# Performance work log

Measured on AMD Instinct MI355X. Metric: run time of the kernel, lower is better.

The kernel has to match this reference:

```python
import jax, jax.numpy as jnp
import numpy as np

WS = 6        # window size -> N = 36 tokens per window
HEADS = 16

def _rel_index(ws):
    coords = np.stack(np.meshgrid(np.arange(ws), np.arange(ws), indexing='ij')).reshape(2, -1)
    rel = coords[:, :, None] - coords[:, None, :] + (ws - 1)
    return jnp.asarray(rel[0] * (2 * ws - 1) + rel[1])  # (N, N) int

REL_IDX = _rel_index(WS)

def _ln(x, g, b, eps=1e-5):
    m = x.mean(-1, keepdims=True)
    v = x.var(-1, keepdims=True)
    return (x - m) / jnp.sqrt(v + eps) * g + b

def setup_inputs() -> dict:
    key = jax.random.key(0)
    ks = jax.random.split(key, 6)
    B, H, W, C = 16, 96, 96, 512
    hid = 4 * C
    s = 0.02
    return {
        'x': jax.random.normal(ks[0], (B, H, W, C), jnp.float32),
        'w_qkv': jax.random.normal(ks[1], (C, 3 * C), jnp.float32) * s,
        'w_proj': jax.random.normal(ks[2], (C, C), jnp.float32) * s,
        'b_proj': jnp.zeros((C,), jnp.float32),
        'rel_bias': jax.random.normal(ks[3], ((2 * WS - 1) ** 2, HEADS), jnp.float32) * s,
        'ln1_g': jnp.ones((C,), jnp.float32), 'ln1_b': jnp.zeros((C,), jnp.float32),
        'ln2_g': jnp.ones((C,), jnp.float32), 'ln2_b': jnp.zeros((C,), jnp.float32),
        'w_fc1': jax.random.normal(ks[4], (C, hid), jnp.float32) * s,
        'b_fc1': jnp.zeros((hid,), jnp.float32),
        'w_fc2': jax.random.normal(ks[5], (hid, C), jnp.float32) * s,
        'b_fc2': jnp.zeros((C,), jnp.float32),
    }

def reference(x, w_qkv, w_proj, b_proj, rel_bias, ln1_g, ln1_b, ln2_g, ln2_b, w_fc1, b_fc1, w_fc2, b_fc2):
    B, H, W, C = x.shape
    h, d, N = HEADS, C // HEADS, WS * WS
    nh, nw = H // WS, W // WS
    # window partition: (B,H,W,C) -> (B*nh*nw, N, C)
    xw = x.reshape(B, nh, WS, nw, WS, C).transpose(0, 1, 3, 2, 4, 5).reshape(B * nh * nw, N, C)
    xn = _ln(xw, ln1_g, ln1_b)
    qkv = xn @ w_qkv
    q, k, v = jnp.split(qkv, 3, axis=-1)
    to_heads = lambda t: t.reshape(-1, N, h, d).transpose(0, 2, 1, 3)  # (B_, h, N, d)
    q = to_heads(q) * (d ** -0.5)
    k = to_heads(k)
    v = to_heads(v)
    attn = jnp.einsum('bhnd,bhmd->bhnm', q, k)
    bias = rel_bias[REL_IDX.reshape(-1)].reshape(N, N, h).transpose(2, 0, 1)  # (h, N, N)
    attn = jax.nn.softmax(attn + bias[None], axis=-1)
    o = jnp.einsum('bhnm,bhmd->bhnd', attn, v).transpose(0, 2, 1, 3).reshape(-1, N, C)
    o = o @ w_proj + b_proj
    # un-window; NOTE: source has no residual around attention (x is replaced)
    x2 = o.reshape(B, nh, nw, WS, WS, C).transpose(0, 1, 3, 2, 4, 5).reshape(B, H, W, C)
    xm = _ln(x2, ln2_g, ln2_b)
    mlp = jax.nn.gelu(xm @ w_fc1 + b_fc1, approximate=False) @ w_fc2 + b_fc2
    return x2 + mlp
```

## Files before the change

kernel.cpp:

```cpp
#include <hip/hip_runtime.h>
#include <stdint.h>

#define TOK 147456
#define CCH 512

typedef __attribute__((ext_vector_type(8))) short short8;
typedef __attribute__((ext_vector_type(4))) float f32x4;

struct alignas(8) US4 { unsigned short a, b, c, d; };

typedef __attribute__((address_space(3))) void lds_void;
typedef const __attribute__((address_space(1))) void gbl_void;

__device__ inline void gload16(const void* g, void* l) {
    __builtin_amdgcn_global_load_lds((gbl_void*)g, (lds_void*)l, 16, 0, 0);
}

__device__ inline unsigned short f2bf(float f) {
    union { float f; unsigned u; } v{f};
    unsigned r = v.u + 0x7fffu + ((v.u >> 16) & 1u);
    return (unsigned short)(r >> 16);
}
__device__ inline float bf2f(unsigned short h) {
    union { unsigned u; float f; } v; v.u = ((unsigned)h) << 16; return v.f;
}

__global__ void wprep(const float* __restrict__ in, unsigned short* __restrict__ out,
                      int K, int N) {
    int idx = blockIdx.x * 256 + threadIdx.x;
    if (idx >= K * N) return;
    int k = idx / N, n = idx % N;
    out[(size_t)n * K + k] = f2bf(in[idx]);
}

__global__ void biasprep(const float* __restrict__ rb, float* __restrict__ bb) {
    int idx = blockIdx.x * 256 + threadIdx.x;
    if (idx >= 16 * 48 * 48) return;
    int h = idx / 2304, rem = idx % 2304, r = rem / 48, c = rem % 48;
    float v = -1e9f;
    if (r < 36 && c < 36) {
        int dy = r / 6 - c / 6 + 5;
        int dx = r % 6 - c % 6 + 5;
        v = rb[(dy * 11 + dx) * 16 + h];
    }
    bb[idx] = v;
}

__global__ __launch_bounds__(256) void ln_k(const float* __restrict__ x,
                                            const float* __restrict__ g,
                                            const float* __restrict__ b,
                                            unsigned short* __restrict__ out, int ntok) {
    int lane = threadIdx.x & 63;
    int tok = blockIdx.x * 4 + (threadIdx.x >> 6);
    if (tok >= ntok) return;
    const float4* xr = (const float4*)(x + (size_t)tok * CCH);
    float4 v0 = xr[lane], v1 = xr[lane + 64];
    float s  = v0.x + v0.y + v0.z + v0.w + v1.x + v1.y + v1.z + v1.w;
    float s2 = v0.x*v0.x + v0.y*v0.y + v0.z*v0.z + v0.w*v0.w
             + v1.x*v1.x + v1.y*v1.y + v1.z*v1.z + v1.w*v1.w;
#pragma unroll
    for (int off = 32; off; off >>= 1) { s += __shfl_xor(s, off); s2 += __shfl_xor(s2, off); }
    float mean = s * (1.f / 512.f);
    float var  = s2 * (1.f / 512.f) - mean * mean;
    float inv  = rsqrtf(var + 1e-5f);
    const float4* gp = (const float4*)g;
    const float4* bp = (const float4*)b;
    float4 g0 = gp[lane], g1 = gp[lane + 64], b0 = bp[lane], b1 = bp[lane + 64];
    US4 o0, o1;
    o0.a = f2bf((v0.x - mean) * inv * g0.x + b0.x);
    o0.b = f2bf((v0.y - mean) * inv * g0.y + b0.y);
    o0.c = f2bf((v0.z - mean) * inv * g0.z + b0.z);
    o0.d = f2bf((v0.w - mean) * inv * g0.w + b0.w);
    o1.a = f2bf((v1.x - mean) * inv * g1.x + b1.x);
    o1.b = f2bf((v1.y - mean) * inv * g1.y + b1.y);
    o1.c = f2bf((v1.z - mean) * inv * g1.z + b1.z);
    o1.d = f2bf((v1.w - mean) * inv * g1.w + b1.w);
    unsigned short* op = out + (size_t)tok * CCH;
    *(US4*)(op + 4 * lane)       = o0;
    *(US4*)(op + 256 + 4 * lane) = o1;
}

__global__ __launch_bounds__(256) void attn_mfma(const unsigned short* __restrict__ qkv,
                                                 const float* __restrict__ biasb,
                                                 unsigned short* __restrict__ o) {
    __shared__ __align__(16) unsigned short p_lds[4][48 * 64];
    __shared__ __align__(16) unsigned short v_lds[4][32 * 64];

    int tid  = threadIdx.x;
    int wv   = tid >> 6;
    int lane = tid & 63;
    int l15  = lane & 15;
    int g    = lane >> 4;

    int wid = blockIdx.x * 4 + wv;
    int h   = wid & 15;
    int win = wid >> 4;
    int img  = win >> 8;
    int wrow = (win >> 4) & 15;
    int wcol = win & 15;
    int tok_base = (img * 96 + wrow * 6) * 96 + wcol * 6;

    unsigned short* pw = p_lds[wv];
    unsigned short* vw = v_lds[wv];

    #define TOKOF(r) (tok_base + (r) + 90 * ((r) / 6))

    short8 z8 = {};
    for (int e = lane; e < 224; e += 64) {
        if (e < 128) {
            int ch = e >> 2, kst = 32 + (e & 3) * 8;
            *(short8*)(vw + ch * 64 + (kst ^ ((ch & 7) << 3))) = z8;
        } else {
            int ee = e - 128; int q = ee >> 1, kst = 48 + (ee & 1) * 8;
            *(short8*)(pw + q * 64 + (kst ^ ((q & 7) << 3))) = z8;
        }
    }

    for (int e = lane; e < 144; e += 64) {
        int r = e >> 2, c0 = (e & 3) * 8;
        short8 vv = *(const short8*)(qkv + (size_t)TOKOF(r) * 1536 + 1024 + h * 32 + c0);
#pragma unroll
        for (int j = 0; j < 8; ++j) {
            int ch = c0 + j;
            vw[ch * 64 + (r ^ ((ch & 7) << 3))] = (unsigned short)vv[j];
        }
    }

    short8 qf[3], kf[3];
#pragma unroll
    for (int t = 0; t < 3; ++t) {
        int r = t * 16 + l15;
        if (r < 36) {
            size_t ba = (size_t)TOKOF(r) * 1536 + h * 32 + g * 8;
            qf[t] = *(const short8*)(qkv + ba);
            kf[t] = *(const short8*)(qkv + ba + 512);
        } else { qf[t] = z8; kf[t] = z8; }
    }

    f32x4 s[3][3] = {};
#pragma unroll
    for (int mt = 0; mt < 3; ++mt)
#pragma unroll
        for (int nt = 0; nt < 3; ++nt)
            s[mt][nt] = __builtin_amdgcn_mfma_f32_16x16x32_bf16(qf[mt], kf[nt], s[mt][nt], 0, 0, 0);

    const float SCALE = 0.17677669529663687f;
    const float* bh = biasb + h * 2304;
#pragma unroll
    for (int mt = 0; mt < 3; ++mt) {
#pragma unroll
        for (int r = 0; r < 4; ++r) {
            int row = mt * 16 + g * 4 + r;
            const float* bb = bh + row * 48 + l15;
            float v0 = fmaf(s[mt][0][r], SCALE, bb[0]);
            float v1 = fmaf(s[mt][1][r], SCALE, bb[16]);
            float v2 = fmaf(s[mt][2][r], SCALE, bb[32]);
            float m = fmaxf(fmaxf(v0, v1), v2);
#pragma unroll
            for (int off = 1; off < 16; off <<= 1) m = fmaxf(m, __shfl_xor(m, off));
            float e0 = __expf(v0 - m), e1 = __expf(v1 - m), e2 = __expf(v2 - m);
            float sm = e0 + e1 + e2;
#pragma unroll
            for (int off = 1; off < 16; off <<= 1) sm += __shfl_xor(sm, off);
            float inv = 1.f / sm;
            int sw = (row & 7) << 3;
            unsigned short* pr = pw + row * 64;
            pr[(l15)      ^ sw] = f2bf(e0 * inv);
            pr[(16 + l15) ^ sw] = f2bf(e1 * inv);
            pr[(32 + l15) ^ sw] = f2bf(e2 * inv);
        }
    }

    f32x4 oacc[3][2] = {};
#pragma unroll
    for (int ks = 0; ks < 2; ++ks) {
        int kst = ks * 32 + g * 8;
        short8 bfr[2];
#pragma unroll
        for (int nt = 0; nt < 2; ++nt) {
            int c = nt * 16 + l15;
            bfr[nt] = *(const short8*)(vw + c * 64 + (kst ^ ((c & 7) << 3)));
        }
#pragma unroll
        for (int mt = 0; mt < 3; ++mt) {
            int q = mt * 16 + l15;
            short8 pa = *(const short8*)(pw + q * 64 + (kst ^ ((q & 7) << 3)));
#pragma unroll
            for (int nt = 0; nt < 2; ++nt)
                oacc[mt][nt] = __builtin_amdgcn_mfma_f32_16x16x32_bf16(pa, bfr[nt], oacc[mt][nt], 0, 0, 0);
        }
    }

#pragma unroll
    for (int mt = 0; mt < 3; ++mt) {
#pragma unroll
        for (int r = 0; r < 4; ++r) {
            int q = mt * 16 + g * 4 + r;
            if (q < 36) {
                size_t rb = (size_t)TOKOF(q) * 512 + h * 32;
#pragma unroll
                for (int nt = 0; nt < 2; ++nt)
                    o[rb + nt * 16 + l15] = f2bf(oacc[mt][nt][r]);
            }
        }
    }
    #undef TOKOF
}

template <int EPI>
__global__ __launch_bounds__(512, 2) void gemm8(const unsigned short* __restrict__ A,
                                                const unsigned short* __restrict__ Bt,
                                                int M, int N, int K,
                                                const float* __restrict__ bias,
                                                const float* __restrict__ resid,
                                                void* __restrict__ Cout) {
    extern __shared__ char lds[];
    int tid = threadIdx.x;
    int w = tid >> 6, lane = tid & 63;
    int l15 = lane & 15, grp = lane >> 4;
    int wm = w >> 2, wn = w & 3;

    int nbn = N >> 8;
    int nwg = gridDim.x;
    int q = nwg >> 3, r = nwg & 7;
    int xcd = blockIdx.x & 7, pos = blockIdx.x >> 3;
    int wgid = (xcd < r ? xcd * (q + 1) : r * (q + 1) + (xcd - r) * q) + pos;
    int bm = wgid / nbn, bn = wgid % nbn;

    int NSLOT = K >> 5;

    int srow = w * 32 + (lane >> 2);
    int g0 = (lane & 3) ^ ((srow >> 1) & 3);
    const unsigned short* aSrc = A  + (size_t)(bm * 256 + srow) * K + g0 * 8;
    const unsigned short* bSrc = Bt + (size_t)(bn * 256 + srow) * K + g0 * 8;
    int ldst = w * 2048 + lane * 16;

    #define STAGE(s) { \
        size_t ko = (size_t)(s) * 32; \
        char* sb_ = lds + ((s) & 3) * 32768; \
        gload16(aSrc + ko, sb_ + ldst); \
        gload16(aSrc + ko + (size_t)16 * K, sb_ + ldst + 1024); \
        gload16(bSrc + ko, sb_ + 16384 + ldst); \
        gload16(bSrc + ko + (size_t)16 * K, sb_ + 16384 + ldst + 1024); \
    }

    int gpos = grp ^ ((l15 >> 1) & 3);
    int aoff = (wm * 128 + l15) * 64 + gpos * 16;
    int boff = 16384 + (wn * 64 + l15) * 64 + gpos * 16;

    f32x4 acc[8][4] = {};

    STAGE(0); STAGE(1); STAGE(2);

    for (int s = 0; s < NSLOT; ++s) {
        int ahead = NSLOT - 1 - s;
        if (ahead >= 3) {
            STAGE(s + 3);
            asm volatile("s_waitcnt vmcnt(12)" ::: "memory");
        } else if (ahead == 2) {
            asm volatile("s_waitcnt vmcnt(8)" ::: "memory");
        } else if (ahead == 1) {
            asm volatile("s_waitcnt vmcnt(4)" ::: "memory");
        } else {
            asm volatile("s_waitcnt vmcnt(0)" ::: "memory");
        }
        asm volatile("s_barrier" ::: "memory");
        char* sb = lds + (s & 3) * 32768;
        short8 af[8], bf4[4];
#pragma unroll
        for (int m = 0; m < 8; ++m) af[m] = *(const short8*)(sb + aoff + m * 1024);
#pragma unroll
        for (int n = 0; n < 4; ++n) bf4[n] = *(const short8*)(sb + boff + n * 1024);
        asm volatile("s_waitcnt lgkmcnt(0)" ::: "memory");
        asm volatile("s_barrier" ::: "memory");
        __builtin_amdgcn_sched_barrier(0);
        __builtin_amdgcn_s_setprio(1);
#pragma unroll
        for (int m = 0; m < 8; ++m)
#pragma unroll
            for (int n = 0; n < 4; ++n)
                acc[m][n] = __builtin_amdgcn_mfma_f32_16x16x32_bf16(af[m], bf4[n], acc[m][n], 0, 0, 0);
        __builtin_amdgcn_s_setprio(0);
    }
    #undef STAGE

    int row0 = bm * 256 + wm * 128 + grp * 4;
    int col0 = bn * 256 + wn * 64 + l15;
#pragma unroll
    for (int m = 0; m < 8; ++m) {
#pragma unroll
        for (int n = 0; n < 4; ++n) {
            int col = col0 + n * 16;
            float bv = (EPI == 0) ? 0.f : bias[col];
#pragma unroll
            for (int r2 = 0; r2 < 4; ++r2) {
                int row = row0 + m * 16 + r2;
                size_t idx = (size_t)row * N + col;
                float val = acc[m][n][r2] + bv;
                if (EPI == 0) {
                    ((unsigned short*)Cout)[idx] = f2bf(val);
                } else if (EPI == 1) {
                    ((float*)Cout)[idx] = val;
                } else if (EPI == 2) {
                    float ge = 0.5f * val * (1.f + erff(val * 0.70710678118654752f));
                    ((unsigned short*)Cout)[idx] = f2bf(ge);
                } else {
                    ((float*)Cout)[idx] = val + resid[idx];
                }
            }
        }
    }
}

extern "C" void kernel_launch(void* const* d_in, const int* in_sizes, int n_in,
                              void* d_out, int out_size, void* d_ws, size_t ws_size,
                              hipStream_t stream) {
    const float* x       = (const float*)d_in[0];
    const float* w_qkv   = (const float*)d_in[1];
    const float* w_proj  = (const float*)d_in[2];
    const float* b_proj  = (const float*)d_in[3];
    const float* relb    = (const float*)d_in[4];
    const float* ln1g    = (const float*)d_in[5];
    const float* ln1b    = (const float*)d_in[6];
    const float* ln2g    = (const float*)d_in[7];
    const float* ln2b    = (const float*)d_in[8];
    const float* w_fc1   = (const float*)d_in[9];
    const float* b_fc1   = (const float*)d_in[10];
    const float* w_fc2   = (const float*)d_in[11];
    const float* b_fc2   = (const float*)d_in[12];
    float* out = (float*)d_out;

    hipFuncSetAttribute(reinterpret_cast<const void*>(&gemm8<0>),
                        hipFuncAttributeMaxDynamicSharedMemorySize, 131072);
    hipFuncSetAttribute(reinterpret_cast<const void*>(&gemm8<1>),
                        hipFuncAttributeMaxDynamicSharedMemorySize, 131072);
    hipFuncSetAttribute(reinterpret_cast<const void*>(&gemm8<2>),
                        hipFuncAttributeMaxDynamicSharedMemorySize, 131072);
    hipFuncSetAttribute(reinterpret_cast<const void*>(&gemm8<3>),
                        hipFuncAttributeMaxDynamicSharedMemorySize, 131072);

    char* w = (char*)d_ws;
    unsigned short* wT_qkv  = (unsigned short*)w; w += (size_t)1536 * 512 * 2;
    unsigned short* wT_proj = (unsigned short*)w; w += (size_t)512  * 512 * 2;
    unsigned short* wT_fc1  = (unsigned short*)w; w += (size_t)2048 * 512 * 2;
    unsigned short* wT_fc2  = (unsigned short*)w; w += (size_t)512  * 2048 * 2;
    float* biasb            = (float*)w;          w += (size_t)16 * 48 * 48 * 4;
    size_t wbytes = (size_t)(w - (char*)d_ws);

    int nchunk = 16;
    for (int c = 1; c <= 16; c *= 2) {
        size_t tokc = TOK / c;
        if (wbytes + tokc * 1024 + tokc * 4096 <= ws_size) { nchunk = c; break; }
    }
    size_t tokc = TOK / nchunk;
    unsigned short* buf1 = (unsigned short*)w;
    unsigned short* buf2 = (unsigned short*)(w + tokc * 1024);

    wprep<<<(512 * 1536 + 255) / 256, 256, 0, stream>>>(w_qkv,  wT_qkv,  512, 1536);
    wprep<<<(512 * 512  + 255) / 256, 256, 0, stream>>>(w_proj, wT_proj, 512, 512);
    wprep<<<(512 * 2048 + 255) / 256, 256, 0, stream>>>(w_fc1,  wT_fc1,  512, 2048);
    wprep<<<(2048 * 512 + 255) / 256, 256, 0, stream>>>(w_fc2,  wT_fc2,  2048, 512);
    biasprep<<<(16 * 48 * 48 + 255) / 256, 256, 0, stream>>>(relb, biasb);

    int Mc = (int)tokc;
    int gm = Mc / 256;
    int imgs = Mc / 9216;

    for (int c = 0; c < nchunk; ++c) {
        size_t toff = (size_t)c * tokc;
        const float* xc = x + toff * CCH;
        float* outc = out + toff * CCH;

        ln_k<<<Mc / 4, 256, 0, stream>>>(xc, ln1g, ln1b, buf1, Mc);
        gemm8<0><<<gm * 6, 512, 131072, stream>>>(buf1, wT_qkv, Mc, 1536, 512,
                                                  nullptr, nullptr, buf2);
        attn_mfma<<<imgs * 1024, 256, 0, stream>>>(buf2, biasb, buf1);
        gemm8<1><<<gm * 2, 512, 131072, stream>>>(buf1, wT_proj, Mc, 512, 512,
                                                  b_proj, nullptr, outc);
        ln_k<<<Mc / 4, 256, 0, stream>>>(outc, ln2g, ln2b, buf1, Mc);
        gemm8<2><<<gm * 8, 512, 131072, stream>>>(buf1, wT_fc1, Mc, 2048, 512,
                                                  b_fc1, nullptr, buf2);
        gemm8<3><<<gm * 2, 512, 131072, stream>>>(buf2, wT_fc2, Mc, 512, 2048,
                                                  b_fc2, outc, outc);
    }
}
```

Measured before the change: 1.867 ms.

## Split GEMM main loop into half-phases, keep proj output in bf16, tanh GELU

Reworks the GEMM mainloop so global-to-LDS staging of A and B is interleaved with two half-tile MFMA phases, using a new XOR swizzle and barrier placement. The launch-bounds occupancy hint drops from 2 to 1. The attention projection now writes bf16 to a scratch buffer instead of fp32 to the output. A new bf16-input LayerNorm kernel reads that buffer, and the final residual reads bf16. The exact erf GELU is replaced by the tanh approximation via exp. These cut memory traffic and epilogue cost, but add bf16 rounding on the residual path and an approximate GELU, which may affect accuracy.

Result: faster. 1.682 ms (-10.0%).

```diff
diff --git a/kernel.cpp b/kernel.cpp
--- a/kernel.cpp
+++ b/kernel.cpp
@@ -80,6 +80,36 @@
     *(US4*)(op + 256 + 4 * lane) = o1;
 }
 
+__global__ __launch_bounds__(256) void ln_bf(const unsigned short* __restrict__ x,
+                                             const float* __restrict__ g,
+                                             const float* __restrict__ b,
+                                             unsigned short* __restrict__ out, int ntok) {
+    int lane = threadIdx.x & 63;
+    int tok = blockIdx.x * 4 + (threadIdx.x >> 6);
+    if (tok >= ntok) return;
+    short8 v = *(const short8*)(x + (size_t)tok * CCH + lane * 8);
+    float f[8];
+#pragma unroll
+    for (int j = 0; j < 8; ++j) f[j] = bf2f((unsigned short)v[j]);
+    float s = 0.f, s2 = 0.f;
+#pragma unroll
+    for (int j = 0; j < 8; ++j) { s += f[j]; s2 += f[j] * f[j]; }
+#pragma unroll
+    for (int off = 32; off; off >>= 1) { s += __shfl_xor(s, off); s2 += __shfl_xor(s2, off); }
+    float mean = s * (1.f / 512.f);
+    float var  = s2 * (1.f / 512.f) - mean * mean;
+    float inv  = rsqrtf(var + 1e-5f);
+    const float4* gp = (const float4*)g + lane * 2;
+    const float4* bp = (const float4*)b + lane * 2;
+    float4 g0 = gp[0], g1 = gp[1], b0 = bp[0], b1 = bp[1];
+    float gg[8] = {g0.x, g0.y, g0.z, g0.w, g1.x, g1.y, g1.z, g1.w};
+    float bb[8] = {b0.x, b0.y, b0.z, b0.w, b1.x, b1.y, b1.z, b1.w};
+    short8 o;
+#pragma unroll
+    for (int j = 0; j < 8; ++j) o[j] = (short)f2bf((f[j] - mean) * inv * gg[j] + bb[j]);
+    *(short8*)(out + (size_t)tok * CCH + lane * 8) = o;
+}
+
 __global__ __launch_bounds__(256) void attn_mfma(const unsigned short* __restrict__ qkv,
                                                  const float* __restrict__ biasb,
                                                  unsigned short* __restrict__ o) {
@@ -208,11 +238,11 @@
 }
 
 template <int EPI>
-__global__ __launch_bounds__(512, 2) void gemm8(const unsigned short* __restrict__ A,
+__global__ __launch_bounds__(512, 1) void gemm8(const unsigned short* __restrict__ A,
                                                 const unsigned short* __restrict__ Bt,
                                                 int M, int N, int K,
                                                 const float* __restrict__ bias,
-                                                const float* __restrict__ resid,
+                                                const unsigned short* __restrict__ resid,
                                                 void* __restrict__ Cout) {
     extern __shared__ char lds[];
     int tid = threadIdx.x;
@@ -223,66 +253,76 @@
     int nbn = N >> 8;
     int nwg = gridDim.x;
     int q = nwg >> 3, r = nwg & 7;
-    int xcd = blockIdx.x & 7, pos = blockIdx.x >> 3;
-    int wgid = (xcd < r ? xcd * (q + 1) : r * (q + 1) + (xcd - r) * q) + pos;
+    int xcd = blockIdx.x & 7, pos_ = blockIdx.x >> 3;
+    int wgid = (xcd < r ? xcd * (q + 1) : r * (q + 1) + (xcd - r) * q) + pos_;
     int bm = wgid / nbn, bn = wgid % nbn;
 
-    int NSLOT = K >> 5;
-
-    int srow = w * 32 + (lane >> 2);
-    int g0 = (lane & 3) ^ ((srow >> 1) & 3);
-    const unsigned short* aSrc = A  + (size_t)(bm * 256 + srow) * K + g0 * 8;
-    const unsigned short* bSrc = Bt + (size_t)(bn * 256 + srow) * K + g0 * 8;
-    int ldst = w * 2048 + lane * 16;
-
-    #define STAGE(s) { \
-        size_t ko = (size_t)(s) * 32; \
-        char* sb_ = lds + ((s) & 3) * 32768; \
-        gload16(aSrc + ko, sb_ + ldst); \
-        gload16(aSrc + ko + (size_t)16 * K, sb_ + ldst + 1024); \
-        gload16(bSrc + ko, sb_ + 16384 + ldst); \
-        gload16(bSrc + ko + (size_t)16 * K, sb_ + 16384 + ldst + 1024); \
-    }
-
-    int gpos = grp ^ ((l15 >> 1) & 3);
-    int aoff = (wm * 128 + l15) * 64 + gpos * 16;
-    int boff = 16384 + (wn * 64 + l15) * 64 + gpos * 16;
+    int NT = K >> 5;
+
+    int u = (tid & 7) ^ ((tid >> 3) & 7);
+    int srow = ((tid >> 3) << 1) + (u >> 2);
+    int scol = (u & 3) * 8;
+    const unsigned short* aSrc = A  + ((size_t)bm * 256 + srow) * (size_t)K + scol;
+    const unsigned short* bSrc = Bt + ((size_t)bn * 256 + srow) * (size_t)K + scol;
+
+    #define STAGE_A(t) do { char* s_ = lds + ((t) & 3) * 32768; size_t ko_ = (size_t)(t) * 32; \
+        gload16(aSrc + ko_, s_ + tid * 16); \
+        gload16(aSrc + ko_ + (size_t)128 * K, s_ + 8192 + tid * 16); } while (0)
+    #define STAGE_B(t) do { char* s_ = lds + ((t) & 3) * 32768 + 16384; size_t ko_ = (size_t)(t) * 32; \
+        gload16(bSrc + ko_, s_ + tid * 16); \
+        gload16(bSrc + ko_ + (size_t)128 * K, s_ + 8192 + tid * 16); } while (0)
+
+    int rpos = (grp + (l15 & 1) * 4) ^ (l15 >> 1);
+    int aRd = (wm * 64 + (l15 >> 1)) * 128 + rpos * 16;
+    int bRd = 16384 + (wn * 32 + (l15 >> 1)) * 128 + rpos * 16;
 
     f32x4 acc[8][4] = {};
 
-    STAGE(0); STAGE(1); STAGE(2);
-
-    for (int s = 0; s < NSLOT; ++s) {
-        int ahead = NSLOT - 1 - s;
-        if (ahead >= 3) {
-            STAGE(s + 3);
-            asm volatile("s_waitcnt vmcnt(12)" ::: "memory");
-        } else if (ahead == 2) {
-            asm volatile("s_waitcnt vmcnt(8)" ::: "memory");
-        } else if (ahead == 1) {
-            asm volatile("s_waitcnt vmcnt(4)" ::: "memory");
-        } else {
-            asm volatile("s_waitcnt vmcnt(0)" ::: "memory");
-        }
-        asm volatile("s_barrier" ::: "memory");
-        char* sb = lds + (s & 3) * 32768;
-        short8 af[8], bf4[4];
-#pragma unroll
-        for (int m = 0; m < 8; ++m) af[m] = *(const short8*)(sb + aoff + m * 1024);
-#pragma unroll
-        for (int n = 0; n < 4; ++n) bf4[n] = *(const short8*)(sb + boff + n * 1024);
+    STAGE_A(0); STAGE_B(0); STAGE_A(1); STAGE_B(1); STAGE_A(2); STAGE_B(2);
+    asm volatile("s_waitcnt vmcnt(8)" ::: "memory");
+    __builtin_amdgcn_s_barrier();
+
+    for (int t = 0; t < NT; ++t) {
+        char* sb = lds + (t & 3) * 32768;
+        short8 af[4], bf[4], ag[4];
+
+#pragma unroll
+        for (int m = 0; m < 4; ++m) af[m] = *(const short8*)(sb + aRd + m * 1024);
+#pragma unroll
+        for (int n = 0; n < 4; ++n) bf[n] = *(const short8*)(sb + bRd + n * 1024);
+        if (t + 3 < NT) STAGE_A(t + 3);
         asm volatile("s_waitcnt lgkmcnt(0)" ::: "memory");
-        asm volatile("s_barrier" ::: "memory");
         __builtin_amdgcn_sched_barrier(0);
         __builtin_amdgcn_s_setprio(1);
 #pragma unroll
-        for (int m = 0; m < 8; ++m)
+        for (int m = 0; m < 4; ++m)
 #pragma unroll
             for (int n = 0; n < 4; ++n)
-                acc[m][n] = __builtin_amdgcn_mfma_f32_16x16x32_bf16(af[m], bf4[n], acc[m][n], 0, 0, 0);
+                acc[m][n] = __builtin_amdgcn_mfma_f32_16x16x32_bf16(af[m], bf[n], acc[m][n], 0, 0, 0);
         __builtin_amdgcn_s_setprio(0);
-    }
-    #undef STAGE
+        __builtin_amdgcn_s_barrier();
+
+#pragma unroll
+        for (int m = 0; m < 4; ++m) ag[m] = *(const short8*)(sb + aRd + (m + 4) * 1024);
+        if (t + 3 < NT) STAGE_B(t + 3);
+        if (t + 1 < NT) {
+            if (t + 3 < NT)      asm volatile("s_waitcnt vmcnt(8)" ::: "memory");
+            else if (t + 2 < NT) asm volatile("s_waitcnt vmcnt(4)" ::: "memory");
+            else                 asm volatile("s_waitcnt vmcnt(0)" ::: "memory");
+        }
+        asm volatile("s_waitcnt lgkmcnt(0)" ::: "memory");
+        __builtin_amdgcn_sched_barrier(0);
+        __builtin_amdgcn_s_setprio(1);
+#pragma unroll
+        for (int m = 0; m < 4; ++m)
+#pragma unroll
+            for (int n = 0; n < 4; ++n)
+                acc[m + 4][n] = __builtin_amdgcn_mfma_f32_16x16x32_bf16(ag[m], bf[n], acc[m + 4][n], 0, 0, 0);
+        __builtin_amdgcn_s_setprio(0);
+        __builtin_amdgcn_s_barrier();
+    }
+    #undef STAGE_A
+    #undef STAGE_B
 
     int row0 = bm * 256 + wm * 128 + grp * 4;
     int col0 = bn * 256 + wn * 64 + l15;
@@ -300,12 +340,16 @@
                 if (EPI == 0) {
                     ((unsigned short*)Cout)[idx] = f2bf(val);
                 } else if (EPI == 1) {
-                    ((float*)Cout)[idx] = val;
+                    ((unsigned short*)Cout)[idx] = f2bf(val);
                 } else if (EPI == 2) {
-                    float ge = 0.5f * val * (1.f + erff(val * 0.70710678118654752f));
+                    float u3 = val * val * val;
+                    float z2 = 1.5957691216f * (val + 0.044715f * u3);
+                    float e = __expf(z2);
+                    float th = 1.f - 2.f / (e + 1.f);
+                    float ge = 0.5f * val * (1.f + th);
                     ((unsigned short*)Cout)[idx] = f2bf(ge);
                 } else {
-                    ((float*)Cout)[idx] = val + resid[idx];
+                    ((float*)Cout)[idx] = val + bf2f(resid[idx]);
                 }
             }
         }
@@ -350,11 +394,12 @@
     int nchunk = 16;
     for (int c = 1; c <= 16; c *= 2) {
         size_t tokc = TOK / c;
-        if (wbytes + tokc * 1024 + tokc * 4096 <= ws_size) { nchunk = c; break; }
+        if (wbytes + tokc * 6144 <= ws_size) { nchunk = c; break; }
     }
     size_t tokc = TOK / nchunk;
     unsigned short* buf1 = (unsigned short*)w;
     unsigned short* buf2 = (unsigned short*)(w + tokc * 1024);
+    unsigned short* buf3 = (unsigned short*)(w + tokc * 5120);
 
     wprep<<<(512 * 1536 + 255) / 256, 256, 0, stream>>>(w_qkv,  wT_qkv,  512, 1536);
     wprep<<<(512 * 512  + 255) / 256, 256, 0, stream>>>(w_proj, wT_proj, 512, 512);
@@ -376,11 +421,11 @@
                                                   nullptr, nullptr, buf2);
         attn_mfma<<<imgs * 1024, 256, 0, stream>>>(buf2, biasb, buf1);
         gemm8<1><<<gm * 2, 512, 131072, stream>>>(buf1, wT_proj, Mc, 512, 512,
-                                                  b_proj, nullptr, outc);
-        ln_k<<<Mc / 4, 256, 0, stream>>>(outc, ln2g, ln2b, buf1, Mc);
+                                                  b_proj, nullptr, buf3);
+        ln_bf<<<Mc / 4, 256, 0, stream>>>(buf3, ln2g, ln2b, buf1, Mc);
         gemm8<2><<<gm * 8, 512, 131072, stream>>>(buf1, wT_fc1, Mc, 2048, 512,
                                                   b_fc1, nullptr, buf2);
         gemm8<3><<<gm * 2, 512, 131072, stream>>>(buf2, wT_fc2, Mc, 512, 2048,
-                                                  b_fc2, outc, outc);
-    }
-}
+                                                  b_fc2, buf3, outc);
+    }
+}
```
